# Kernel tuning notes

Measured on AMD Instinct MI355X. Metric: run time of the kernel, lower is better.

The kernel has to match this reference:

```python
import jax, jax.numpy as jnp
import numpy as np

N_HEADS = 4
N_HIDDEN = 64  # out_features // n_heads
NEG_SLOPE = 0.2


def setup_inputs() -> dict:
    key = jax.random.key(0)
    k1, k2, k3, k4, k5 = jax.random.split(key, 5)
    B, N, F_IN, F_OUT = 1, 4096, 128, 256
    h = jax.random.normal(k1, (B, N, F_IN), dtype=jnp.float32)
    adj_mat = jax.random.uniform(k2, (N, N, 1), dtype=jnp.float32)
    W_proj = jax.random.normal(k3, (F_IN, N_HEADS * N_HIDDEN), dtype=jnp.float32) / np.sqrt(F_IN)
    W_proj_attn = jax.random.normal(k4, (F_IN, N_HEADS * N_HIDDEN // 2), dtype=jnp.float32) / np.sqrt(F_IN)
    w_attn = jax.random.normal(k5, (N_HIDDEN,), dtype=jnp.float32) / np.sqrt(N_HIDDEN)
    return {"h": h, "adj_mat": adj_mat, "W_proj": W_proj, "W_proj_attn": W_proj_attn, "w_attn": w_attn}


def reference(h, adj_mat, W_proj, W_proj_attn, w_attn):
    B, N, _ = h.shape
    H, D = N_HEADS, N_HIDDEN
    half = D // 2
    # value projection: (B, N, H, D)
    g = (h @ W_proj).reshape(B, N, H, D)
    # attention-feature projection: (B, N, H, D//2)
    ga = (h @ W_proj_attn).reshape(B, N, H, half)
    # attn(cat([ga_i, ga_j])) decomposes linearly: e_ij = <w_l, ga_i> + <w_r, ga_j>
    # (identical math to the torch repeat/cat/Linear, without the NxNxD tensor)
    el = jnp.einsum('bnhk,k->bnh', ga, w_attn[:half])   # dest node i term
    er = jnp.einsum('bnhk,k->bnh', ga, w_attn[half:])   # source node j term
    e = jax.nn.leaky_relu(el[:, :, None, :] + er[:, None, :, :], NEG_SLOPE)  # (B, N, N, H)
    mask = adj_mat >= 0.5  # (N, N, 1) broadcasts over (B, N, N, H)
    e = jnp.where(mask, e, -jnp.inf)
    a = jax.nn.softmax(e, axis=2)  # softmax over source nodes j
    # dropout is identity in eval mode
    out = jnp.einsum('bijh,bjhf->bihf', a, g)  # (B, N, H, D)
    return out.reshape(B, N, H * D)  # is_concat=True
```

## Files before the change

### kernel.cpp

```cpp
#include <hip/hip_runtime.h>
#include <hip/hip_bf16.h>

typedef __bf16 bf16_t;
typedef __bf16 bf16x4 __attribute__((ext_vector_type(4)));
typedef __bf16 bf16x8 __attribute__((ext_vector_type(8)));
typedef float floatx4 __attribute__((ext_vector_type(4)));

#define N_NODES 4096
#define F_IN 128
#define NUM_HEADS 4
#define D_HID 64
#define F_OUT 256
#define NEG_SLOPE 0.2f

__global__ __launch_bounds__(384) void proj_kernel(
    const float* __restrict__ hmat, const float* __restrict__ Wp,
    const float* __restrict__ Wa, const float* __restrict__ wattn,
    bf16_t* __restrict__ GB, float* __restrict__ el,
    float* __restrict__ E1r, float* __restrict__ E2r)
{
    __shared__ float hl[4][F_IN];
    const int t = threadIdx.x;
    const int j0 = blockIdx.x * 4;

    if (t < 128) {
        const int jl = t >> 5, m0 = (t & 31) * 4;
        *reinterpret_cast<float4*>(&hl[jl][m0]) =
            *reinterpret_cast<const float4*>(&hmat[(size_t)(j0 + jl) * F_IN + m0]);
    }
    __syncthreads();

    float acc[4] = {0.f, 0.f, 0.f, 0.f};

    const float* wptr;
    int stride;
    if (t < 256) { wptr = Wp + t;         stride = 256; }
    else         { wptr = Wa + (t - 256); stride = 128; }

    for (int m = 0; m < F_IN; m += 4) {
        const float w0 = wptr[(size_t)(m + 0) * stride];
        const float w1 = wptr[(size_t)(m + 1) * stride];
        const float w2 = wptr[(size_t)(m + 2) * stride];
        const float w3 = wptr[(size_t)(m + 3) * stride];
#pragma unroll
        for (int jl = 0; jl < 4; ++jl) {
            const float4 hv = *reinterpret_cast<const float4*>(&hl[jl][m]);
            acc[jl] = fmaf(hv.w, w3, fmaf(hv.z, w2, fmaf(hv.y, w1, fmaf(hv.x, w0, acc[jl]))));
        }
    }

    if (t < 256) {
        const int h = t >> 6, f = t & 63;
        bf16x4 o;
#pragma unroll
        for (int q = 0; q < 4; ++q) o[q] = (bf16_t)acc[q];
        const size_t base = ((((size_t)h * 128 + (j0 >> 5)) * 4 + (f >> 4)) * 64
                             + (f & 15) + 16 * ((j0 >> 3) & 3)) * 8 + (j0 & 7);
        *reinterpret_cast<bf16x4*>(&GB[base]) = o;
    } else {
        const int ta = t - 256;
        const int ha = ta >> 5, k = ta & 31;
        const float wl = wattn[k], wr = wattn[32 + k];
#pragma unroll
        for (int jl = 0; jl < 4; ++jl) {
            float vl = acc[jl] * wl;
            float vr = acc[jl] * wr;
#pragma unroll
            for (int s = 16; s >= 1; s >>= 1) {
                vl += __shfl_xor(vl, s, 64);
                vr += __shfl_xor(vr, s, 64);
            }
            if (k == 0) {
                el[ha * N_NODES + j0 + jl]  = vl;
                E1r[ha * N_NODES + j0 + jl] = __expf(vr);
                E2r[ha * N_NODES + j0 + jl] = __expf(NEG_SLOPE * vr);
            }
        }
    }
}

__global__ __launch_bounds__(256, 4) void attn_kernel(
    const float* __restrict__ adj, const bf16_t* __restrict__ GB,
    const float* __restrict__ el, const float* __restrict__ E1r,
    const float* __restrict__ E2r,
    float* __restrict__ numout, float* __restrict__ den_g,
    int njc, int ntiles)
{
    __shared__ float adj_s[2][16 * 68];

    const int tid = threadIdx.x;
    const int i0  = blockIdx.x * 16;
    const int jc  = blockIdx.y;
    const int jT0 = jc * ntiles * 64;

    const int r = tid >> 4;
    const int c = tid & 15;

    const int hh   = tid >> 6;
    const int lane = tid & 63;
    const int m    = lane & 15;
    const int quad = lane >> 4;

    const float eli = el[hh * N_NODES + i0 + m];
    const float E1i = __expf(eli);
    const float E2i = __expf(NEG_SLOPE * eli);
    const float Ti  = __expf(-eli);

    const float* adjp = adj + (size_t)(i0 + r) * N_NODES + c * 4;

    floatx4 acc0 = {0.f, 0.f, 0.f, 0.f};
    floatx4 acc1 = acc0, acc2 = acc0, acc3 = acc0, accd = acc0;
    bf16x8 ones;
#pragma unroll
    for (int q = 0; q < 8; ++q) ones[q] = (bf16_t)1.0f;

    float4 adjv = *reinterpret_cast<const float4*>(adjp + jT0);
    *reinterpret_cast<float4*>(&adj_s[0][r * 68 + c * 4]) = adjv;
    if (ntiles > 1)
        adjv = *reinterpret_cast<const float4*>(adjp + jT0 + 64);
    __syncthreads();

    for (int k = 0; k < ntiles; ++k) {
        const int buf = k & 1;
        const int jT  = jT0 + k * 64;

        if (k + 1 < ntiles) {
            *reinterpret_cast<float4*>(&adj_s[buf ^ 1][r * 68 + c * 4]) = adjv;
            if (k + 2 < ntiles)
                adjv = *reinterpret_cast<const float4*>(adjp + jT + 128);
        }

        const float*  E1p = E1r + hh * N_NODES + jT + quad * 8;
        const float*  E2p = E2r + hh * N_NODES + jT + quad * 8;
        const bf16_t* gbb = GB + (size_t)(hh * 128 + (jT >> 5)) * 2048 + lane * 8;

#pragma unroll
        for (int kt = 0; kt < 2; ++kt) {
            const float4 e1a = *reinterpret_cast<const float4*>(E1p + kt * 32);
            const float4 e1b = *reinterpret_cast<const float4*>(E1p + kt * 32 + 4);
            const float4 e2a = *reinterpret_cast<const float4*>(E2p + kt * 32);
            const float4 e2b = *reinterpret_cast<const float4*>(E2p + kt * 32 + 4);
            const float4 aa  = *reinterpret_cast<const float4*>(
                &adj_s[buf][m * 68 + kt * 32 + quad * 8]);
            const float4 ab  = *reinterpret_cast<const float4*>(
                &adj_s[buf][m * 68 + kt * 32 + quad * 8 + 4]);

            bf16x8 af;
            af[0] = (aa.x >= 0.5f) ? (bf16_t)((e1a.x > Ti) ? E1i * e1a.x : E2i * e2a.x) : (bf16_t)0.f;
            af[1] = (aa.y >= 0.5f) ? (bf16_t)((e1a.y > Ti) ? E1i * e1a.y : E2i * e2a.y) : (bf16_t)0.f;
            af[2] = (aa.z >= 0.5f) ? (bf16_t)((e1a.z > Ti) ? E1i * e1a.z : E2i * e2a.z) : (bf16_t)0.f;
            af[3] = (aa.w >= 0.5f) ? (bf16_t)((e1a.w > Ti) ? E1i * e1a.w : E2i * e2a.w) : (bf16_t)0.f;
            af[4] = (ab.x >= 0.5f) ? (bf16_t)((e1b.x > Ti) ? E1i * e1b.x : E2i * e2b.x) : (bf16_t)0.f;
            af[5] = (ab.y >= 0.5f) ? (bf16_t)((e1b.y > Ti) ? E1i * e1b.y : E2i * e2b.y) : (bf16_t)0.f;
            af[6] = (ab.z >= 0.5f) ? (bf16_t)((e1b.z > Ti) ? E1i * e1b.z : E2i * e2b.z) : (bf16_t)0.f;
            af[7] = (ab.w >= 0.5f) ? (bf16_t)((e1b.w > Ti) ? E1i * e1b.w : E2i * e2b.w) : (bf16_t)0.f;

            const bf16x8 b0 = *reinterpret_cast<const bf16x8*>(gbb + kt * 2048);
            const bf16x8 b1 = *reinterpret_cast<const bf16x8*>(gbb + kt * 2048 + 512);
            const bf16x8 b2 = *reinterpret_cast<const bf16x8*>(gbb + kt * 2048 + 1024);
            const bf16x8 b3 = *reinterpret_cast<const bf16x8*>(gbb + kt * 2048 + 1536);

            accd = __builtin_amdgcn_mfma_f32_16x16x32_bf16(af, ones, accd, 0, 0, 0);
            acc0 = __builtin_amdgcn_mfma_f32_16x16x32_bf16(af, b0, acc0, 0, 0, 0);
            acc1 = __builtin_amdgcn_mfma_f32_16x16x32_bf16(af, b1, acc1, 0, 0, 0);
            acc2 = __builtin_amdgcn_mfma_f32_16x16x32_bf16(af, b2, acc2, 0, 0, 0);
            acc3 = __builtin_amdgcn_mfma_f32_16x16x32_bf16(af, b3, acc3, 0, 0, 0);
        }
        __syncthreads();
    }

    const int ibase = i0 + quad * 4;
    if (njc == 1) {
#pragma unroll
        for (int rr = 0; rr < 4; ++rr) {
            const float rd = 1.0f / accd[rr];
            float* dst = numout + (size_t)(ibase + rr) * F_OUT + hh * D_HID + m;
            dst[0]  = acc0[rr] * rd;
            dst[16] = acc1[rr] * rd;
            dst[32] = acc2[rr] * rd;
            dst[48] = acc3[rr] * rd;
        }
    } else {
        float* nrow = numout + (size_t)jc * ((size_t)N_NODES * F_OUT);
#pragma unroll
        for (int rr = 0; rr < 4; ++rr) {
            float* dst = nrow + (size_t)(ibase + rr) * F_OUT + hh * D_HID + m;
            dst[0]  = acc0[rr];
            dst[16] = acc1[rr];
            dst[32] = acc2[rr];
            dst[48] = acc3[rr];
        }
        if (m == 0) {
#pragma unroll
            for (int rr = 0; rr < 4; ++rr)
                den_g[((size_t)jc * N_NODES + ibase + rr) * NUM_HEADS + hh] = accd[rr];
        }
    }
}

__global__ __launch_bounds__(256) void reduce_kernel(
    const float* __restrict__ num, const float* __restrict__ den,
    float* __restrict__ out, int njc)
{
    const int idx = blockIdx.x * 256 + threadIdx.x;
    const int i  = idx >> 8;
    const int c  = idx & 255;
    const int hh = c >> 6;
    float n = 0.f, d = 0.f;
    for (int jc = 0; jc < njc; ++jc) {
        n += num[(size_t)jc * ((size_t)N_NODES * F_OUT) + idx];
        d += den[((size_t)jc * N_NODES + i) * NUM_HEADS + hh];
    }
    out[idx] = n / d;
}

extern "C" void kernel_launch(void* const* d_in, const int* in_sizes, int n_in,
                              void* d_out, int out_size, void* d_ws, size_t ws_size,
                              hipStream_t stream)
{
    const float* hmat = (const float*)d_in[0];
    const float* adj  = (const float*)d_in[1];
    const float* Wp   = (const float*)d_in[2];
    const float* Wa   = (const float*)d_in[3];
    const float* watt = (const float*)d_in[4];
    float* out = (float*)d_out;

    char* ws = (char*)d_ws;
    bf16_t* GB  = (bf16_t*)ws;
    float*  el  = (float*)(ws + (2ull << 20));
    float*  E1r = (float*)(ws + (2ull << 20) + (64ull << 10));
    float*  E2r = (float*)(ws + (2ull << 20) + (128ull << 10));
    const size_t baseoff = (2ull << 20) + (192ull << 10);

    const size_t num_bytes = (size_t)N_NODES * F_OUT * 4;
    const size_t den_bytes = (size_t)N_NODES * NUM_HEADS * 4;
    const int njc = (ws_size >= baseoff + 4 * (num_bytes + den_bytes)) ? 4 : 2;

    float* num = (float*)(ws + baseoff);
    float* den = (float*)(ws + baseoff + (size_t)njc * num_bytes);

    proj_kernel<<<1024, 384, 0, stream>>>(hmat, Wp, Wa, watt, GB, el, E1r, E2r);
    attn_kernel<<<dim3(256, njc), 256, 0, stream>>>(adj, GB, el, E1r, E2r,
                                                    num, den, njc, (N_NODES / njc) / 64);
    reduce_kernel<<<(N_NODES * F_OUT) / 256, 256, 0, stream>>>(num, den, out, njc);
}
```

Measured before the change: 163.4 us.

## Load adjacency directly from global per wave instead of LDS double buffer

Removes the shared-memory double-buffered staging of the adjacency tile and its per-iteration barrier. Each wave now reads its adjacency row segments straight from global memory, so the four head-waves each fetch the same adjacency data (4x redundant global/L2 traffic on the dominant 64MB input). The inner loop is unrolled by two and the pointer setup is hoisted. It trades barrier and LDS overhead for duplicated loads that rely on cache hits.

```diff
diff --git a/kernel.cpp b/kernel.cpp
--- a/kernel.cpp
+++ b/kernel.cpp
@@ -86,16 +86,11 @@
     float* __restrict__ numout, float* __restrict__ den_g,
     int njc, int ntiles)
 {
-    __shared__ float adj_s[2][16 * 68];
-
     const int tid = threadIdx.x;
     const int i0  = blockIdx.x * 16;
     const int jc  = blockIdx.y;
     const int jT0 = jc * ntiles * 64;
 
-    const int r = tid >> 4;
-    const int c = tid & 15;
-
     const int hh   = tid >> 6;
     const int lane = tid & 63;
     const int m    = lane & 15;
@@ -106,7 +101,10 @@
     const float E2i = __expf(NEG_SLOPE * eli);
     const float Ti  = __expf(-eli);
 
-    const float* adjp = adj + (size_t)(i0 + r) * N_NODES + c * 4;
+    const float* adjl = adj + (size_t)(i0 + m) * N_NODES + quad * 8;
+    const float* E1p  = E1r + hh * N_NODES + quad * 8;
+    const float* E2p  = E2r + hh * N_NODES + quad * 8;
+    const bf16_t* gb0 = GB + (size_t)hh * 128 * 2048 + lane * 8;
 
     floatx4 acc0 = {0.f, 0.f, 0.f, 0.f};
     floatx4 acc1 = acc0, acc2 = acc0, acc3 = acc0, accd = acc0;
@@ -114,36 +112,20 @@
 #pragma unroll
     for (int q = 0; q < 8; ++q) ones[q] = (bf16_t)1.0f;
 
-    float4 adjv = *reinterpret_cast<const float4*>(adjp + jT0);
-    *reinterpret_cast<float4*>(&adj_s[0][r * 68 + c * 4]) = adjv;
-    if (ntiles > 1)
-        adjv = *reinterpret_cast<const float4*>(adjp + jT0 + 64);
-    __syncthreads();
-
+#pragma unroll 2
     for (int k = 0; k < ntiles; ++k) {
-        const int buf = k & 1;
-        const int jT  = jT0 + k * 64;
-
-        if (k + 1 < ntiles) {
-            *reinterpret_cast<float4*>(&adj_s[buf ^ 1][r * 68 + c * 4]) = adjv;
-            if (k + 2 < ntiles)
-                adjv = *reinterpret_cast<const float4*>(adjp + jT + 128);
-        }
-
-        const float*  E1p = E1r + hh * N_NODES + jT + quad * 8;
-        const float*  E2p = E2r + hh * N_NODES + jT + quad * 8;
-        const bf16_t* gbb = GB + (size_t)(hh * 128 + (jT >> 5)) * 2048 + lane * 8;
+        const int jT = jT0 + k * 64;
+        const bf16_t* gbb = gb0 + (size_t)(jT >> 5) * 2048;
 
 #pragma unroll
         for (int kt = 0; kt < 2; ++kt) {
-            const float4 e1a = *reinterpret_cast<const float4*>(E1p + kt * 32);
-            const float4 e1b = *reinterpret_cast<const float4*>(E1p + kt * 32 + 4);
-            const float4 e2a = *reinterpret_cast<const float4*>(E2p + kt * 32);
-            const float4 e2b = *reinterpret_cast<const float4*>(E2p + kt * 32 + 4);
-            const float4 aa  = *reinterpret_cast<const float4*>(
-                &adj_s[buf][m * 68 + kt * 32 + quad * 8]);
-            const float4 ab  = *reinterpret_cast<const float4*>(
-                &adj_s[buf][m * 68 + kt * 32 + quad * 8 + 4]);
+            const int jk = jT + kt * 32;
+            const float4 aa  = *reinterpret_cast<const float4*>(adjl + jk);
+            const float4 ab  = *reinterpret_cast<const float4*>(adjl + jk + 4);
+            const float4 e1a = *reinterpret_cast<const float4*>(E1p + jk);
+            const float4 e1b = *reinterpret_cast<const float4*>(E1p + jk + 4);
+            const float4 e2a = *reinterpret_cast<const float4*>(E2p + jk);
+            const float4 e2b = *reinterpret_cast<const float4*>(E2p + jk + 4);
 
             bf16x8 af;
             af[0] = (aa.x >= 0.5f) ? (bf16_t)((e1a.x > Ti) ? E1i * e1a.x : E2i * e2a.x) : (bf16_t)0.f;
@@ -166,7 +148,6 @@
             acc2 = __builtin_amdgcn_mfma_f32_16x16x32_bf16(af, b2, acc2, 0, 0, 0);
             acc3 = __builtin_amdgcn_mfma_f32_16x16x32_bf16(af, b3, acc3, 0, 0, 0);
         }
-        __syncthreads();
     }
 
     const int ibase = i0 + quad * 4;
```

Measured after the change: 179.3 us. +9.7%, slower.
